# Kernel tuning notes

Measured on AMD Instinct MI355X. Metric: run time of the kernel, lower is better.

Reference implementation:

```python
import jax, jax.numpy as jnp
import numpy as np

N, M, E, D = 20000, 1024, 640000, 256


def setup_inputs() -> dict:
    key = jax.random.key(0)
    ks = jax.random.split(key, 24)
    mask = jax.random.uniform(ks[0], (N, M)) < 0.05
    init = jnp.where(mask, jax.random.uniform(ks[1], (N, M), minval=0.1, maxval=1.0), 0.0)
    inp = {
        'init': init,
        'ei_cc': jax.random.randint(ks[2], (2, E), 0, N, dtype=jnp.int32),
        'ei_cac': jax.random.randint(ks[3], (2, E), 0, N, dtype=jnp.int32),
        'ei_csc': jax.random.randint(ks[4], (2, E), 0, N, dtype=jnp.int32),
        'ea_cc': jax.random.uniform(ks[5], (E,), minval=0.1, maxval=1.0),
        'ea_cac': jax.random.uniform(ks[6], (E,), minval=0.1, maxval=1.0),
        'ea_csc': jax.random.uniform(ks[7], (E,), minval=0.1, maxval=1.0),
        # Projection MLP: Linear(1,16) -> ReLU -> Linear(16,D)
        'pW1': jax.random.normal(ks[8], (1, 16)) * 0.5,
        'pb1': jnp.zeros((16,)),
        'pW2': jax.random.normal(ks[9], (16, D)) * 0.1,
        'pb2': jnp.zeros((D,)),
        # three GCN branches, 3 layers each (all D->D)
        'W_cc': jax.random.normal(ks[10], (3, D, D)) * 0.05,
        'b_cc': jnp.zeros((3, D)),
        'W_cac': jax.random.normal(ks[11], (3, D, D)) * 0.05,
        'b_cac': jnp.zeros((3, D)),
        'W_csc': jax.random.normal(ks[12], (3, D, D)) * 0.05,
        'b_csc': jnp.zeros((3, D)),
        # meta-path attention: Linear(D, 1)
        'w_att': jax.random.normal(ks[13], (D,)) * 0.05,
        'b_att': jnp.zeros((1,)),
    }
    return inp


def projection(init, pW1, pb1, pW2, pb2):
    # torch code feeds the *indices* of nonzero columns through the MLP and
    # mean-pools per row. Vectorize: precompute MLP(j) for every column index j,
    # then masked mean.
    idx = jnp.arange(M, dtype=init.dtype)[:, None]          # [M, 1]
    h = jax.nn.relu(idx @ pW1 + pb1)                        # [M, 16]
    col_emb = h @ pW2 + pb2                                 # [M, D]
    mask = (init != 0).astype(init.dtype)                   # [N, M]
    cnt = mask.sum(axis=1)                                  # [N]
    emb = (mask @ col_emb) / jnp.maximum(cnt, 1.0)[:, None]
    return jnp.where(cnt[:, None] > 0, emb, 0.0)            # zero rows stay zero


def gcn_conv(x, edge_index, edge_weight, W, b):
    # PyG GCNConv with edge_weight: add self loops (w=1), symmetric norm.
    n = x.shape[0]
    loop = jnp.arange(n, dtype=edge_index.dtype)
    row = jnp.concatenate([edge_index[0], loop])
    col = jnp.concatenate([edge_index[1], loop])
    w = jnp.concatenate([edge_weight, jnp.ones((n,), x.dtype)])
    deg = jax.ops.segment_sum(w, col, num_segments=n)
    dinv = jnp.where(deg > 0, jax.lax.rsqrt(deg), 0.0)
    norm = dinv[row] * w * dinv[col]                        # [E+N]
    h = x @ W                                               # [N, D]
    out = jax.ops.segment_sum(norm[:, None] * h[row], col, num_segments=n)
    return out + b


def gcn_branch(x, edge_index, edge_weight, Ws, bs):
    for l in range(3):
        x = jax.nn.relu(gcn_conv(x, edge_index, edge_weight, Ws[l], bs[l]))
    return x


def reference(init, ei_cc, ei_cac, ei_csc, ea_cc, ea_cac, ea_csc,
              pW1, pb1, pW2, pb2, W_cc, b_cc, W_cac, b_cac, W_csc, b_csc,
              w_att, b_att):
    x0 = projection(init, pW1, pb1, pW2, pb2)               # [N, D]
    out_cc = gcn_branch(x0, ei_cc, ea_cc, W_cc, b_cc)
    out_cac = gcn_branch(x0, ei_cac, ea_cac, W_cac, b_cac)
    out_csc = gcn_branch(x0, ei_csc, ea_csc, W_csc, b_csc)
    emb = jnp.stack([out_cc, out_cac, out_csc], axis=0)     # [3, N, D]
    scores = jnp.einsum('pnd,d->pn', emb, w_att) + b_att[0] # [3, N]
    attn = jax.nn.softmax(scores, axis=0)                   # softmax over meta-paths
    return jnp.einsum('pn,pnd->nd', attn, emb)              # [N, D]
```

## Files before the change

### kernel.cpp

```cpp
#include <hip/hip_runtime.h>
#include <hip/hip_bf16.h>

typedef __hip_bfloat16 bf16;
typedef __bf16 v8bf __attribute__((ext_vector_type(8)));
typedef float f32x4 __attribute__((ext_vector_type(4)));
typedef unsigned int v4u __attribute__((ext_vector_type(4)));

constexpr int N = 20000, M = 1024, E = 640000, D = 256;
constexpr size_t SEGEL = (size_t)N * D;
constexpr int NCHUNK = 10000;
constexpr int NSLICE = 64;
constexpr int ESLICE = E / NSLICE;

__device__ __forceinline__ float b2f(bf16 v) { return __bfloat162float(v); }
__device__ __forceinline__ bf16 f2b(float f) { return __float2bfloat16(f); }
__device__ __forceinline__ float u2f(unsigned short u) { return __uint_as_float(((unsigned)u) << 16); }
__device__ __forceinline__ unsigned short f2u(float f) { bf16 h = __float2bfloat16(f); return *(unsigned short*)&h; }
__device__ __forceinline__ float loadf(const void* p, size_t i, int isbf) {
    return isbf ? b2f(((const bf16*)p)[i]) : ((const float*)p)[i];
}
__device__ __forceinline__ void fma8(float* acc, uint4 v, float w) {
    acc[0] = fmaf(w, u2f((unsigned short)(v.x & 0xffffu)), acc[0]);
    acc[1] = fmaf(w, u2f((unsigned short)(v.x >> 16)), acc[1]);
    acc[2] = fmaf(w, u2f((unsigned short)(v.y & 0xffffu)), acc[2]);
    acc[3] = fmaf(w, u2f((unsigned short)(v.y >> 16)), acc[3]);
    acc[4] = fmaf(w, u2f((unsigned short)(v.z & 0xffffu)), acc[4]);
    acc[5] = fmaf(w, u2f((unsigned short)(v.z >> 16)), acc[5]);
    acc[6] = fmaf(w, u2f((unsigned short)(v.w & 0xffffu)), acc[6]);
    acc[7] = fmaf(w, u2f((unsigned short)(v.w >> 16)), acc[7]);
}
__device__ __forceinline__ void add4(float* acc, uint2 v) {
    acc[0] += u2f((unsigned short)(v.x & 0xffffu));
    acc[1] += u2f((unsigned short)(v.x >> 16));
    acc[2] += u2f((unsigned short)(v.y & 0xffffu));
    acc[3] += u2f((unsigned short)(v.y >> 16));
}
__device__ __forceinline__ unsigned pack2(float a, float b) {
    return (unsigned)f2u(a) | ((unsigned)f2u(b) << 16);
}

__global__ void detect_kernel(const void* __restrict__ ea, int* __restrict__ flag)
{
    if (threadIdx.x == 0 && blockIdx.x == 0) {
        const unsigned short* u = (const unsigned short*)ea;
        int cnt = 0;
        for (int i = 0; i < 64; i++) {
            float f = __uint_as_float(((unsigned)u[i]) << 16);
            if (f >= 0.05f && f <= 1.05f) cnt++;
        }
        *flag = (cnt >= 60) ? 1 : 0;
    }
}

__global__ __launch_bounds__(256) void prep_kernel(
    const void* __restrict__ W0, const void* __restrict__ W1, const void* __restrict__ W2,
    const void* __restrict__ pW1, const void* __restrict__ pb1,
    const void* __restrict__ pW2, const void* __restrict__ pb2,
    bf16* __restrict__ WT, bf16* __restrict__ cemb, const int* __restrict__ flag)
{
    int isbf = *flag;
    int b = blockIdx.x;
    if (b < 2304) {
        int mat = b >> 8, n = b & 255, k = threadIdx.x;
        const void* W = (mat < 3) ? W0 : (mat < 6) ? W1 : W2;
        int lm = mat - (mat < 3 ? 0 : (mat < 6 ? 3 : 6));
        WT[(size_t)mat * 65536 + n * 256 + k] =
            f2b(loadf(W, (size_t)lm * 65536 + k * 256 + n, isbf));
    } else {
        int j = b - 2304;
        int d = threadIdx.x;
        float jf = (float)j;
        float acc = loadf(pb2, d, isbf);
        #pragma unroll
        for (int k = 0; k < 16; k++) {
            float h = fmaxf(jf * loadf(pW1, k, isbf) + loadf(pb1, k, isbf), 0.0f);
            acc += h * loadf(pW2, k * 256 + d, isbf);
        }
        cemb[(size_t)j * 256 + d] = f2b(acc);
    }
}

__global__ __launch_bounds__(256) void projection_kernel(
    const void* __restrict__ init, const bf16* __restrict__ cemb,
    bf16* __restrict__ x0, const int* __restrict__ flag)
{
    __shared__ unsigned short idxs[4][1024];
    int isbf = *flag;
    int wave = threadIdx.x >> 6, lane = threadIdx.x & 63;
    int i = blockIdx.x * 4 + wave;
    unsigned long long below = (lane == 63) ? 0x7fffffffffffffffull
                                            : ((1ull << lane) - 1ull);
    int cnt = 0;
    if (isbf) {
        const unsigned short* row = (const unsigned short*)init + (size_t)i * 1024;
        for (int c0 = 0; c0 < 1024; c0 += 64) {
            bool nz = (row[c0 + lane] & 0x7fffu) != 0;
            unsigned long long m = __ballot(nz);
            if (nz) idxs[wave][cnt + __popcll(m & below)] = (unsigned short)(c0 + lane);
            cnt += __popcll(m);
        }
    } else {
        const float* row = (const float*)init + (size_t)i * 1024;
        for (int c0 = 0; c0 < 1024; c0 += 64) {
            bool nz = row[c0 + lane] != 0.0f;
            unsigned long long m = __ballot(nz);
            if (nz) idxs[wave][cnt + __popcll(m & below)] = (unsigned short)(c0 + lane);
            cnt += __popcll(m);
        }
    }
    const uint2* cr = (const uint2*)cemb;
    float acc[4] = {0.0f, 0.0f, 0.0f, 0.0f};
    int j = 0;
    for (; j + 8 <= cnt; j += 8) {
        uint2 v0 = cr[(size_t)idxs[wave][j + 0] * 64 + lane];
        uint2 v1 = cr[(size_t)idxs[wave][j + 1] * 64 + lane];
        uint2 v2 = cr[(size_t)idxs[wave][j + 2] * 64 + lane];
        uint2 v3 = cr[(size_t)idxs[wave][j + 3] * 64 + lane];
        uint2 v4 = cr[(size_t)idxs[wave][j + 4] * 64 + lane];
        uint2 v5 = cr[(size_t)idxs[wave][j + 5] * 64 + lane];
        uint2 v6 = cr[(size_t)idxs[wave][j + 6] * 64 + lane];
        uint2 v7 = cr[(size_t)idxs[wave][j + 7] * 64 + lane];
        add4(acc, v0); add4(acc, v1); add4(acc, v2); add4(acc, v3);
        add4(acc, v4); add4(acc, v5); add4(acc, v6); add4(acc, v7);
    }
    for (; j < cnt; j++) {
        uint2 v = cr[(size_t)idxs[wave][j] * 64 + lane];
        add4(acc, v);
    }
    float rinv = 1.0f / fmaxf((float)cnt, 1.0f);
    uint2 o;
    o.x = pack2(acc[0] * rinv, acc[1] * rinv);
    o.y = pack2(acc[2] * rinv, acc[3] * rinv);
    ((uint2*)x0)[(size_t)i * 64 + lane] = o;
}

__global__ __launch_bounds__(256) void countP_kernel(
    const int* __restrict__ e0, const int* __restrict__ e1, const int* __restrict__ e2,
    int* __restrict__ P)
{
    __shared__ int cur[NCHUNK];
    int b = blockIdx.x;
    int pb = b >> 7, rem = b & 127;
    int ck = rem >> 6, s = rem & 63;
    const int* ei = pb == 0 ? e0 : pb == 1 ? e1 : e2;
    int c0 = ck * NCHUNK;
    int t = threadIdx.x;
    for (int i = t; i < NCHUNK; i += 256) cur[i] = 0;
    __syncthreads();
    int ebase = s * ESLICE;
    for (int e = ebase + t; e < ebase + ESLICE; e += 256) {
        int c = ei[E + e];
        if (c >= c0 && c < c0 + NCHUNK) atomicAdd(&cur[c - c0], 1);
    }
    __syncthreads();
    int* Prow = P + ((size_t)(pb * NSLICE + s)) * N + c0;
    for (int i = t; i < NCHUNK; i += 256) Prow[i] = cur[i];
}

__global__ __launch_bounds__(256) void cnt_sum_kernel(
    const int* __restrict__ P, int* __restrict__ cnt)
{
    int id = blockIdx.x * 256 + threadIdx.x;
    if (id >= 3 * N) return;
    int pb = id / N, c = id - pb * N;
    int sum = 0;
    #pragma unroll 8
    for (int s = 0; s < NSLICE; s++)
        sum += P[((size_t)(pb * NSLICE + s)) * N + c];
    cnt[id] = sum;
}

__global__ __launch_bounds__(1024) void scan_kernel(
    const int* __restrict__ cnt, int* __restrict__ col_ptr)
{
    int pb = blockIdx.x;
    int base = pb * E;
    __shared__ int s[1024];
    int t = threadIdx.x;
    const int CH = 20;
    int i0 = t * CH;
    int sum = 0;
    for (int j = 0; j < CH; j++) { int i = i0 + j; if (i < N) sum += cnt[pb * N + i]; }
    s[t] = sum;
    __syncthreads();
    for (int off = 1; off < 1024; off <<= 1) {
        int v = (t >= off) ? s[t - off] : 0;
        __syncthreads();
        s[t] += v;
        __syncthreads();
    }
    int run = base + s[t] - sum;
    for (int j = 0; j < CH; j++) {
        int i = i0 + j;
        if (i < N) {
            col_ptr[pb * (N + 1) + i] = run;
            run += cnt[pb * N + i];
        }
    }
    if (t == 0) col_ptr[pb * (N + 1) + N] = base + E;
}

__global__ __launch_bounds__(256) void base_kernel(
    int* __restrict__ P, const int* __restrict__ col_ptr)
{
    int id = blockIdx.x * 256 + threadIdx.x;
    if (id >= 3 * N) return;
    int pb = id / N, c = id - pb * N;
    int run = col_ptr[pb * (N + 1) + c];
    for (int s = 0; s < NSLICE; s++) {
        size_t idx = ((size_t)(pb * NSLICE + s)) * N + c;
        int v = P[idx];
        P[idx] = run;
        run += v;
    }
}

__global__ __launch_bounds__(256) void fill_kernel(
    const int* __restrict__ e0, const int* __restrict__ e1, const int* __restrict__ e2,
    const void* __restrict__ a0, const void* __restrict__ a1, const void* __restrict__ a2,
    const int* __restrict__ P, int2* __restrict__ epack, const int* __restrict__ flag)
{
    __shared__ int cur[NCHUNK];
    int isbf = *flag;
    int b = blockIdx.x;
    int pb = b >> 7, rem = b & 127;
    int ck = rem >> 6, s = rem & 63;
    const int* ei = pb == 0 ? e0 : pb == 1 ? e1 : e2;
    const void* ea = pb == 0 ? a0 : pb == 1 ? a1 : a2;
    int c0 = ck * NCHUNK;
    int t = threadIdx.x;
    const int* Prow = P + ((size_t)(pb * NSLICE + s)) * N + c0;
    for (int i = t; i < NCHUNK; i += 256) cur[i] = Prow[i];
    __syncthreads();
    int ebase = s * ESLICE;
    for (int e = ebase + t; e < ebase + ESLICE; e += 256) {
        int c = ei[E + e];
        if (c >= c0 && c < c0 + NCHUNK) {
            int r = ei[e];
            float w = loadf(ea, e, isbf);
            int pos = atomicAdd(&cur[c - c0], 1);
            int2 v; v.x = r; v.y = __float_as_int(w);
            epack[pos] = v;
        }
    }
}

__global__ __launch_bounds__(256) void degsum_kernel(
    const int* __restrict__ col_ptr, const int2* __restrict__ epack,
    float* __restrict__ dinv, float* __restrict__ nloop)
{
    int wave = threadIdx.x >> 6, lane = threadIdx.x & 63;
    int pb = blockIdx.x / 5000;
    int i = (blockIdx.x - pb * 5000) * 4 + wave;
    int start = col_ptr[pb * (N + 1) + i], end = col_ptr[pb * (N + 1) + i + 1];
    float sum = 0.0f;
    for (int p = start + lane; p < end; p += 64) sum += __int_as_float(epack[p].y);
    for (int off = 1; off < 64; off <<= 1) sum += __shfl_xor(sum, off, 64);
    if (lane == 0) {
        float dg = 1.0f + sum;
        dinv[pb * N + i] = rsqrtf(dg);
        nloop[pb * N + i] = 1.0f / dg;
    }
}

__global__ __launch_bounds__(256) void snorm_sort_kernel(
    const int* __restrict__ col_ptr, int2* __restrict__ epack,
    const float* __restrict__ dinv)
{
    int wave = threadIdx.x >> 6, lane = threadIdx.x & 63;
    int pb = blockIdx.x / 5000;
    int i = (blockIdx.x - pb * 5000) * 4 + wave;
    int start = col_ptr[pb * (N + 1) + i], end = col_ptr[pb * (N + 1) + i + 1];
    float dc = dinv[pb * N + i];
    for (int base = start; base < end; base += 64) {
        int n = end - base; n = n < 64 ? n : 64;
        int key = 0x7fffffff, val = 0;
        if (lane < n) {
            int2 v = epack[base + lane];
            key = v.x;
            val = __float_as_int(dc * __int_as_float(v.y) * dinv[pb * N + v.x]);
        }
        #pragma unroll
        for (int k = 2; k <= 64; k <<= 1) {
            #pragma unroll
            for (int j = k >> 1; j > 0; j >>= 1) {
                int pk = __shfl_xor(key, j, 64);
                int pv = __shfl_xor(val, j, 64);
                bool up = (lane & k) == 0;
                bool lower = (lane & j) == 0;
                bool takeMin = (up == lower);
                bool sw = takeMin ? (pk < key) : (pk > key);
                if (sw) { key = pk; val = pv; }
            }
        }
        if (lane < n) {
            int2 o; o.x = key; o.y = val;
            epack[base + lane] = o;
        }
    }
}

__global__ __launch_bounds__(256) void aggregate_kernel(
    const bf16* __restrict__ xi0, const bf16* __restrict__ xi1, const bf16* __restrict__ xi2,
    bf16* __restrict__ yb,
    const int* __restrict__ col_ptr, const int2* __restrict__ epack,
    const float* __restrict__ nloop)
{
    int wave = threadIdx.x >> 6, lane = threadIdx.x & 63;
    int pb = blockIdx.x / 5000;
    int i = (blockIdx.x - pb * 5000) * 4 + wave;
    const bf16* x = pb == 0 ? xi0 : pb == 1 ? xi1 : xi2;
    const uint4* xr = (const uint4*)x;
    int L = lane & 31, h = lane >> 5;
    int start = col_ptr[pb * (N + 1) + i], end = col_ptr[pb * (N + 1) + i + 1];
    float nl = nloop[pb * N + i];
    float acc[8];
    {
        uint4 sv = xr[(size_t)i * 32 + L];
        float self = (h == 0) ? nl : 0.0f;
        #pragma unroll
        for (int j = 0; j < 8; j++) acc[j] = 0.0f;
        fma8(acc, sv, self);
    }
    for (int base = start; base < end; base += 64) {
        int n = end - base; n = n < 64 ? n : 64;
        int ex = 0, ey = 0;
        if (lane < n) {
            unsigned long long ev = __builtin_nontemporal_load(
                (const unsigned long long*)(epack + base + lane));
            ex = (int)(unsigned)(ev & 0xffffffffull);
            ey = (int)(unsigned)(ev >> 32);
        }
        int pmax = (n + 1) >> 1;
        for (int p0 = 0; p0 < pmax; p0 += 8) {
            int m = pmax - p0; m = m < 8 ? m : 8;
            uint4 v[8];
            float w[8];
            #pragma unroll
            for (int k = 0; k < 8; k++) {
                int e = 2 * (p0 + k) + h;
                int rj = __shfl(ex, e, 64);
                w[k] = __int_as_float(__shfl(ey, e, 64));
                if (k < m) v[k] = xr[(size_t)rj * 32 + L];
            }
            #pragma unroll
            for (int k = 0; k < 8; k++)
                if (k < m) fma8(acc, v[k], w[k]);
        }
    }
    #pragma unroll
    for (int j = 0; j < 8; j++) acc[j] += __shfl_xor(acc[j], 32, 64);
    if (h == 0) {
        v4u o;
        o.x = pack2(acc[0], acc[1]);
        o.y = pack2(acc[2], acc[3]);
        o.z = pack2(acc[4], acc[5]);
        o.w = pack2(acc[6], acc[7]);
        __builtin_nontemporal_store(o,
            (v4u*)yb + (size_t)pb * (SEGEL / 8) + (size_t)i * 32 + L);
    }
}

__global__ __launch_bounds__(256) void gemm_relu_kernel(
    const bf16* __restrict__ yb, const bf16* __restrict__ WT, int layer,
    const void* __restrict__ b0, const void* __restrict__ b1, const void* __restrict__ b2,
    bf16* __restrict__ o0, bf16* __restrict__ o1, bf16* __restrict__ o2,
    const int* __restrict__ flag)
{
    int isbf = *flag;
    int pl = blockIdx.x / 625, blk = blockIdx.x - pl * 625;
    const bf16* y = yb + (size_t)pl * SEGEL;
    const bf16* wt = WT + (size_t)(pl * 3 + layer) * 65536;
    const void* bias = pl == 0 ? b0 : pl == 1 ? b1 : b2;
    bf16* xout = pl == 0 ? o0 : pl == 1 ? o1 : o2;

    int wave = threadIdx.x >> 6, lane = threadIdx.x & 63;
    int m0 = blk * 32 + (wave >> 1) * 16;
    int n0 = (wave & 1) * 128;
    int mrow = lane & 15, q = lane >> 4;

    f32x4 acc[8] = {};
    const v8bf* arow = reinterpret_cast<const v8bf*>(y + (size_t)(m0 + mrow) * 256);
    for (int k0 = 0; k0 < 256; k0 += 32) {
        v8bf a = arow[(k0 >> 3) + q];
        #pragma unroll
        for (int nt = 0; nt < 8; nt++) {
            const v8bf* brow = reinterpret_cast<const v8bf*>(wt + (size_t)(n0 + nt * 16 + mrow) * 256);
            acc[nt] = __builtin_amdgcn_mfma_f32_16x16x32_bf16(a, brow[(k0 >> 3) + q], acc[nt], 0, 0, 0);
        }
    }
    #pragma unroll
    for (int nt = 0; nt < 8; nt++) {
        int col = n0 + nt * 16 + mrow;
        float bv = loadf(bias, (size_t)layer * 256 + col, isbf);
        #pragma unroll
        for (int r = 0; r < 4; r++) {
            int row = m0 + q * 4 + r;
            xout[(size_t)row * 256 + col] = f2b(fmaxf(acc[nt][r] + bv, 0.0f));
        }
    }
}

__global__ __launch_bounds__(256) void attention_kernel(
    const bf16* __restrict__ e0, const bf16* __restrict__ e1, const bf16* __restrict__ e2,
    const void* __restrict__ w_att, void* __restrict__ out, int n_nodes,
    const int* __restrict__ flag)
{
    int isbf = *flag;
    int wave = threadIdx.x >> 6, lane = threadIdx.x & 63;
    int n = blockIdx.x * 4 + wave;
    if (n >= n_nodes) return;
    int d0 = lane * 4;
    float w[4], v0[4], v1[4], v2[4];
    #pragma unroll
    for (int j = 0; j < 4; j++) {
        w[j]  = loadf(w_att, d0 + j, isbf);
        v0[j] = b2f(e0[(size_t)n * 256 + d0 + j]);
        v1[j] = b2f(e1[(size_t)n * 256 + d0 + j]);
        v2[j] = b2f(e2[(size_t)n * 256 + d0 + j]);
    }
    float s0 = 0, s1 = 0, s2 = 0;
    #pragma unroll
    for (int j = 0; j < 4; j++) { s0 += v0[j] * w[j]; s1 += v1[j] * w[j]; s2 += v2[j] * w[j]; }
    for (int off = 1; off < 64; off <<= 1) {
        s0 += __shfl_xor(s0, off, 64);
        s1 += __shfl_xor(s1, off, 64);
        s2 += __shfl_xor(s2, off, 64);
    }
    float m = fmaxf(s0, fmaxf(s1, s2));
    float a0 = expf(s0 - m), a1 = expf(s1 - m), a2 = expf(s2 - m);
    float inv = 1.0f / (a0 + a1 + a2);
    a0 *= inv; a1 *= inv; a2 *= inv;
    #pragma unroll
    for (int j = 0; j < 4; j++) {
        float v = a0 * v0[j] + a1 * v1[j] + a2 * v2[j];
        if (isbf) ((bf16*)out)[(size_t)n * 256 + d0 + j] = f2b(v);
        else      ((float*)out)[(size_t)n * 256 + d0 + j] = v;
    }
}

extern "C" void kernel_launch(void* const* d_in, const int* in_sizes, int n_in,
                              void* d_out, int out_size, void* d_ws, size_t ws_size,
                              hipStream_t stream)
{
    (void)in_sizes; (void)n_in; (void)out_size; (void)ws_size;

    const void* init = d_in[0];
    const int*  ei[3] = {(const int*)d_in[1], (const int*)d_in[2], (const int*)d_in[3]};
    const void* ea[3] = {d_in[4], d_in[5], d_in[6]};
    const void* pW1 = d_in[7];
    const void* pb1 = d_in[8];
    const void* pW2 = d_in[9];
    const void* pb2 = d_in[10];
    const void* Wb[3] = {d_in[11], d_in[13], d_in[15]};
    const void* bb[3] = {d_in[12], d_in[14], d_in[16]};
    const void* w_att = d_in[17];

    char* ws = (char*)d_ws;
    size_t off = 0;
    auto carve = [&](size_t bytes) -> char* {
        off = (off + 255) & ~(size_t)255;
        char* p = ws + off; off += bytes; return p;
    };
    int*   flag  = (int*)carve(4);
    bf16*  WT    = (bf16*)carve((size_t)9 * 65536 * 2);
    bf16*  cemb  = (bf16*)carve((size_t)M * D * 2);
    bf16*  x0    = (bf16*)carve(SEGEL * 2);
    int*   cnt   = (int*)carve((size_t)3 * N * 4);
    int*   colp  = (int*)carve((size_t)3 * (N + 1) * 4);
    float* dinv  = (float*)carve((size_t)3 * N * 4);
    float* nloop = (float*)carve((size_t)3 * N * 4);
    int2*  epack = (int2*)carve((size_t)3 * E * 8);
    bf16*  ybuf  = (bf16*)carve((size_t)3 * SEGEL * 2);
    bf16*  bufA  = (bf16*)carve((size_t)3 * SEGEL * 2);
    bf16*  bufB  = (bf16*)carve((size_t)3 * SEGEL * 2);
    int* P = (int*)bufB;

    detect_kernel<<<1, 64, 0, stream>>>(ea[0], flag);
    prep_kernel<<<3328, 256, 0, stream>>>(Wb[0], Wb[1], Wb[2],
                                          pW1, pb1, pW2, pb2, WT, cemb, flag);
    projection_kernel<<<5000, 256, 0, stream>>>(init, cemb, x0, flag);

    countP_kernel<<<384, 256, 0, stream>>>(ei[0], ei[1], ei[2], P);
    cnt_sum_kernel<<<(3 * N + 255) / 256, 256, 0, stream>>>(P, cnt);
    scan_kernel<<<3, 1024, 0, stream>>>(cnt, colp);
    base_kernel<<<(3 * N + 255) / 256, 256, 0, stream>>>(P, colp);
    fill_kernel<<<384, 256, 0, stream>>>(ei[0], ei[1], ei[2], ea[0], ea[1], ea[2],
                                         P, epack, flag);
    degsum_kernel<<<15000, 256, 0, stream>>>(colp, epack, dinv, nloop);
    snorm_sort_kernel<<<15000, 256, 0, stream>>>(colp, epack, dinv);

    const bf16 *i0 = x0, *i1 = x0, *i2 = x0;
    bf16* dsts[3] = {bufA, bufB, bufA};
    for (int l = 0; l < 3; l++) {
        aggregate_kernel<<<15000, 256, 0, stream>>>(i0, i1, i2, ybuf, colp, epack, nloop);
        bf16* dst = dsts[l];
        gemm_relu_kernel<<<1875, 256, 0, stream>>>(ybuf, WT, l, bb[0], bb[1], bb[2],
                                                   dst, dst + SEGEL, dst + 2 * SEGEL, flag);
        i0 = dst; i1 = dst + SEGEL; i2 = dst + 2 * SEGEL;
    }
    attention_kernel<<<5000, 256, 0, stream>>>(bufA, bufA + SEGEL, bufA + 2 * SEGEL,
                                               w_att, d_out, N, flag);
}
```

Before: 896.9 us.

## Pack edges to 32-bit, widen projection gather, retile GEMM to 128 rows

```diff
diff --git a/kernel.cpp b/kernel.cpp
--- a/kernel.cpp
+++ b/kernel.cpp
@@ -29,11 +29,15 @@
     acc[6] = fmaf(w, u2f((unsigned short)(v.w & 0xffffu)), acc[6]);
     acc[7] = fmaf(w, u2f((unsigned short)(v.w >> 16)), acc[7]);
 }
-__device__ __forceinline__ void add4(float* acc, uint2 v) {
-    acc[0] += u2f((unsigned short)(v.x & 0xffffu));
-    acc[1] += u2f((unsigned short)(v.x >> 16));
-    acc[2] += u2f((unsigned short)(v.y & 0xffffu));
-    acc[3] += u2f((unsigned short)(v.y >> 16));
+__device__ __forceinline__ void add8(float* a, uint4 v) {
+    a[0] += u2f((unsigned short)(v.x & 0xffffu));
+    a[1] += u2f((unsigned short)(v.x >> 16));
+    a[2] += u2f((unsigned short)(v.y & 0xffffu));
+    a[3] += u2f((unsigned short)(v.y >> 16));
+    a[4] += u2f((unsigned short)(v.z & 0xffffu));
+    a[5] += u2f((unsigned short)(v.z >> 16));
+    a[6] += u2f((unsigned short)(v.w & 0xffffu));
+    a[7] += u2f((unsigned short)(v.w >> 16));
 }
 __device__ __forceinline__ unsigned pack2(float a, float b) {
     return (unsigned)f2u(a) | ((unsigned)f2u(b) << 16);
@@ -108,30 +112,42 @@
             cnt += __popcll(m);
         }
     }
-    const uint2* cr = (const uint2*)cemb;
-    float acc[4] = {0.0f, 0.0f, 0.0f, 0.0f};
-    int j = 0;
-    for (; j + 8 <= cnt; j += 8) {
-        uint2 v0 = cr[(size_t)idxs[wave][j + 0] * 64 + lane];
-        uint2 v1 = cr[(size_t)idxs[wave][j + 1] * 64 + lane];
-        uint2 v2 = cr[(size_t)idxs[wave][j + 2] * 64 + lane];
-        uint2 v3 = cr[(size_t)idxs[wave][j + 3] * 64 + lane];
-        uint2 v4 = cr[(size_t)idxs[wave][j + 4] * 64 + lane];
-        uint2 v5 = cr[(size_t)idxs[wave][j + 5] * 64 + lane];
-        uint2 v6 = cr[(size_t)idxs[wave][j + 6] * 64 + lane];
-        uint2 v7 = cr[(size_t)idxs[wave][j + 7] * 64 + lane];
-        add4(acc, v0); add4(acc, v1); add4(acc, v2); add4(acc, v3);
-        add4(acc, v4); add4(acc, v5); add4(acc, v6); add4(acc, v7);
-    }
-    for (; j < cnt; j++) {
-        uint2 v = cr[(size_t)idxs[wave][j] * 64 + lane];
-        add4(acc, v);
-    }
-    float rinv = 1.0f / fmaxf((float)cnt, 1.0f);
-    uint2 o;
-    o.x = pack2(acc[0] * rinv, acc[1] * rinv);
-    o.y = pack2(acc[2] * rinv, acc[3] * rinv);
-    ((uint2*)x0)[(size_t)i * 64 + lane] = o;
+    const uint4* cr4 = (const uint4*)cemb;
+    int L = lane & 31, h = lane >> 5;
+    float acc[8] = {0.f, 0.f, 0.f, 0.f, 0.f, 0.f, 0.f, 0.f};
+    int npair = cnt >> 1;
+    int t = 0;
+    for (; t + 8 <= npair; t += 8) {
+        uint4 v0 = cr4[(size_t)idxs[wave][2 * (t + 0) + h] * 32 + L];
+        uint4 v1 = cr4[(size_t)idxs[wave][2 * (t + 1) + h] * 32 + L];
+        uint4 v2 = cr4[(size_t)idxs[wave][2 * (t + 2) + h] * 32 + L];
+        uint4 v3 = cr4[(size_t)idxs[wave][2 * (t + 3) + h] * 32 + L];
+        uint4 v4 = cr4[(size_t)idxs[wave][2 * (t + 4) + h] * 32 + L];
+        uint4 v5 = cr4[(size_t)idxs[wave][2 * (t + 5) + h] * 32 + L];
+        uint4 v6 = cr4[(size_t)idxs[wave][2 * (t + 6) + h] * 32 + L];
+        uint4 v7 = cr4[(size_t)idxs[wave][2 * (t + 7) + h] * 32 + L];
+        add8(acc, v0); add8(acc, v1); add8(acc, v2); add8(acc, v3);
+        add8(acc, v4); add8(acc, v5); add8(acc, v6); add8(acc, v7);
+    }
+    for (; t < npair; t++) {
+        uint4 v = cr4[(size_t)idxs[wave][2 * t + h] * 32 + L];
+        add8(acc, v);
+    }
+    if ((cnt & 1) && h == 0) {
+        uint4 v = cr4[(size_t)idxs[wave][cnt - 1] * 32 + L];
+        add8(acc, v);
+    }
+    #pragma unroll
+    for (int j = 0; j < 8; j++) acc[j] += __shfl_xor(acc[j], 32, 64);
+    if (h == 0) {
+        float rinv = 1.0f / fmaxf((float)cnt, 1.0f);
+        v4u o;
+        o.x = pack2(acc[0] * rinv, acc[1] * rinv);
+        o.y = pack2(acc[2] * rinv, acc[3] * rinv);
+        o.z = pack2(acc[4] * rinv, acc[5] * rinv);
+        o.w = pack2(acc[6] * rinv, acc[7] * rinv);
+        ((v4u*)x0)[(size_t)i * 32 + L] = o;
+    }
 }
 
 __global__ __launch_bounds__(256) void countP_kernel(
@@ -264,8 +280,8 @@
 }
 
 __global__ __launch_bounds__(256) void snorm_sort_kernel(
-    const int* __restrict__ col_ptr, int2* __restrict__ epack,
-    const float* __restrict__ dinv)
+    const int* __restrict__ col_ptr, const int2* __restrict__ epack,
+    unsigned* __restrict__ epk2, const float* __restrict__ dinv)
 {
     int wave = threadIdx.x >> 6, lane = threadIdx.x & 63;
     int pb = blockIdx.x / 5000;
@@ -294,8 +310,8 @@
             }
         }
         if (lane < n) {
-            int2 o; o.x = key; o.y = val;
-            epack[base + lane] = o;
+            epk2[base + lane] = (unsigned)key
+                              | ((unsigned)f2u(__int_as_float(val)) << 16);
         }
     }
 }
@@ -303,7 +319,7 @@
 __global__ __launch_bounds__(256) void aggregate_kernel(
     const bf16* __restrict__ xi0, const bf16* __restrict__ xi1, const bf16* __restrict__ xi2,
     bf16* __restrict__ yb,
-    const int* __restrict__ col_ptr, const int2* __restrict__ epack,
+    const int* __restrict__ col_ptr, const unsigned* __restrict__ epk2,
     const float* __restrict__ nloop)
 {
     int wave = threadIdx.x >> 6, lane = threadIdx.x & 63;
@@ -324,13 +340,9 @@
     }
     for (int base = start; base < end; base += 64) {
         int n = end - base; n = n < 64 ? n : 64;
-        int ex = 0, ey = 0;
-        if (lane < n) {
-            unsigned long long ev = __builtin_nontemporal_load(
-                (const unsigned long long*)(epack + base + lane));
-            ex = (int)(unsigned)(ev & 0xffffffffull);
-            ey = (int)(unsigned)(ev >> 32);
-        }
+        int ev = 0;
+        if (lane < n)
+            ev = (int)__builtin_nontemporal_load(epk2 + base + lane);
         int pmax = (n + 1) >> 1;
         for (int p0 = 0; p0 < pmax; p0 += 8) {
             int m = pmax - p0; m = m < 8 ? m : 8;
@@ -339,8 +351,9 @@
             #pragma unroll
             for (int k = 0; k < 8; k++) {
                 int e = 2 * (p0 + k) + h;
-                int rj = __shfl(ex, e, 64);
-                w[k] = __int_as_float(__shfl(ey, e, 64));
+                int ee = __shfl(ev, e, 64);
+                int rj = ee & 0xffff;
+                w[k] = u2f((unsigned short)((unsigned)ee >> 16));
                 if (k < m) v[k] = xr[(size_t)rj * 32 + L];
             }
             #pragma unroll
@@ -367,26 +380,40 @@
     bf16* __restrict__ o0, bf16* __restrict__ o1, bf16* __restrict__ o2,
     const int* __restrict__ flag)
 {
+    constexpr int BPL = 157;
     int isbf = *flag;
-    int pl = blockIdx.x / 625, blk = blockIdx.x - pl * 625;
+    int pl = blockIdx.x / BPL, blk = blockIdx.x - pl * BPL;
     const bf16* y = yb + (size_t)pl * SEGEL;
     const bf16* wt = WT + (size_t)(pl * 3 + layer) * 65536;
     const void* bias = pl == 0 ? b0 : pl == 1 ? b1 : b2;
     bf16* xout = pl == 0 ? o0 : pl == 1 ? o1 : o2;
 
     int wave = threadIdx.x >> 6, lane = threadIdx.x & 63;
-    int m0 = blk * 32 + (wave >> 1) * 16;
-    int n0 = (wave & 1) * 128;
+    int wr = wave >> 1, wn = wave & 1;
+    int m0 = blk * 128 + wr * 64;
+    int n0 = wn * 128;
     int mrow = lane & 15, q = lane >> 4;
 
-    f32x4 acc[8] = {};
-    const v8bf* arow = reinterpret_cast<const v8bf*>(y + (size_t)(m0 + mrow) * 256);
+    int ar[4];
+    #pragma unroll
+    for (int rs = 0; rs < 4; rs++) {
+        int r = m0 + rs * 16 + mrow;
+        ar[rs] = r < N ? r : N - 1;
+    }
+
+    f32x4 acc[4][8] = {};
     for (int k0 = 0; k0 < 256; k0 += 32) {
-        v8bf a = arow[(k0 >> 3) + q];
+        int kq = (k0 >> 3) + q;
+        v8bf b[8];
         #pragma unroll
-        for (int nt = 0; nt < 8; nt++) {
-            const v8bf* brow = reinterpret_cast<const v8bf*>(wt + (size_t)(n0 + nt * 16 + mrow) * 256);
-            acc[nt] = __builtin_amdgcn_mfma_f32_16x16x32_bf16(a, brow[(k0 >> 3) + q], acc[nt], 0, 0, 0);
+        for (int nt = 0; nt < 8; nt++)
+            b[nt] = reinterpret_cast<const v8bf*>(wt + (size_t)(n0 + nt * 16 + mrow) * 256)[kq];
+        #pragma unroll
+        for (int rs = 0; rs < 4; rs++) {
+            v8bf a = reinterpret_cast<const v8bf*>(y + (size_t)ar[rs] * 256)[kq];
+            #pragma unroll
+            for (int nt = 0; nt < 8; nt++)
+                acc[rs][nt] = __builtin_amdgcn_mfma_f32_16x16x32_bf16(a, b[nt], acc[rs][nt], 0, 0, 0);
         }
     }
     #pragma unroll
@@ -394,9 +421,13 @@
         int col = n0 + nt * 16 + mrow;
         float bv = loadf(bias, (size_t)layer * 256 + col, isbf);
         #pragma unroll
-        for (int r = 0; r < 4; r++) {
-            int row = m0 + q * 4 + r;
-            xout[(size_t)row * 256 + col] = f2b(fmaxf(acc[nt][r] + bv, 0.0f));
+        for (int rs = 0; rs < 4; rs++) {
+            #pragma unroll
+            for (int r = 0; r < 4; r++) {
+                int row = m0 + rs * 16 + q * 4 + r;
+                if (row < N)
+                    xout[(size_t)row * 256 + col] = f2b(fmaxf(acc[rs][nt][r] + bv, 0.0f));
+            }
         }
     }
 }
@@ -471,6 +502,7 @@
     float* dinv  = (float*)carve((size_t)3 * N * 4);
     float* nloop = (float*)carve((size_t)3 * N * 4);
     int2*  epack = (int2*)carve((size_t)3 * E * 8);
+    unsigned* epk2 = (unsigned*)carve((size_t)3 * E * 4);
     bf16*  ybuf  = (bf16*)carve((size_t)3 * SEGEL * 2);
     bf16*  bufA  = (bf16*)carve((size_t)3 * SEGEL * 2);
     bf16*  bufB  = (bf16*)carve((size_t)3 * SEGEL * 2);
@@ -488,15 +520,15 @@
     fill_kernel<<<384, 256, 0, stream>>>(ei[0], ei[1], ei[2], ea[0], ea[1], ea[2],
                                          P, epack, flag);
     degsum_kernel<<<15000, 256, 0, stream>>>(colp, epack, dinv, nloop);
-    snorm_sort_kernel<<<15000, 256, 0, stream>>>(colp, epack, dinv);
+    snorm_sort_kernel<<<15000, 256, 0, stream>>>(colp, epack, epk2, dinv);
 
     const bf16 *i0 = x0, *i1 = x0, *i2 = x0;
     bf16* dsts[3] = {bufA, bufB, bufA};
     for (int l = 0; l < 3; l++) {
-        aggregate_kernel<<<15000, 256, 0, stream>>>(i0, i1, i2, ybuf, colp, epack, nloop);
+        aggregate_kernel<<<15000, 256, 0, stream>>>(i0, i1, i2, ybuf, colp, epk2, nloop);
         bf16* dst = dsts[l];
-        gemm_relu_kernel<<<1875, 256, 0, stream>>>(ybuf, WT, l, bb[0], bb[1], bb[2],
-                                                   dst, dst + SEGEL, dst + 2 * SEGEL, flag);
+        gemm_relu_kernel<<<3 * 157, 256, 0, stream>>>(ybuf, WT, l, bb[0], bb[1], bb[2],
+                                                      dst, dst + SEGEL, dst + 2 * SEGEL, flag);
         i0 = dst; i1 = dst + SEGEL; i2 = dst + 2 * SEGEL;
     }
     attention_kernel<<<5000, 256, 0, stream>>>(bufA, bufA + SEGEL, bufA + 2 * SEGEL,
```

Measured after the change: 871.1 us. 1.03x faster.
